# Kernel optimization log

Measured on AMD Instinct MI355X. Metric: run time of the kernel, lower is better.

The kernel has to match this reference:

```python
import jax, jax.numpy as jnp
import numpy as np

N = 50000
IN_CH = 128
OUT_CH = 64
H1, C1 = 8, 8


def gat_layer(x, src, dst, W, att_src, att_dst, bias, heads, out_ch, concat, n_nodes):
    # x: [N, F_in]; W: [F_in, heads*out_ch]; att_*: [heads, out_ch]; bias: [heads*out_ch] or [out_ch]
    h = (x @ W).reshape(n_nodes, heads, out_ch)              # [N,H,C]
    a_src = jnp.einsum('nhc,hc->nh', h, att_src)             # [N,H]
    a_dst = jnp.einsum('nhc,hc->nh', h, att_dst)             # [N,H]
    e = jax.nn.leaky_relu(a_src[src] + a_dst[dst], 0.2)      # [E,H]
    # segment softmax over incoming edges of each dst node
    m = jax.ops.segment_max(e, dst, num_segments=n_nodes)    # [N,H]
    p = jnp.exp(e - m[dst])                                  # [E,H]
    s = jax.ops.segment_sum(p, dst, num_segments=n_nodes)    # [N,H]
    alpha = p / (s[dst] + 1e-16)                             # [E,H]
    out = jax.ops.segment_sum(h[src] * alpha[:, :, None], dst, num_segments=n_nodes)  # [N,H,C]
    out = out.reshape(n_nodes, heads * out_ch) if concat else out.mean(axis=1)
    return out + bias


def setup_inputs() -> dict:
    key = jax.random.key(0)
    ks = jax.random.split(key, 12)
    E = 1600000
    x = jax.random.normal(ks[0], (N, IN_CH), dtype=jnp.float32)
    edge_index = jax.random.randint(ks[1], (2, E), 0, N, dtype=jnp.int64)
    sc = 0.1
    return {
        'x': x,
        'edge_index': edge_index,
        'W1': jax.random.normal(ks[2], (IN_CH, H1 * C1), dtype=jnp.float32) * sc,
        'att_src1': jax.random.normal(ks[3], (H1, C1), dtype=jnp.float32) * sc,
        'att_dst1': jax.random.normal(ks[4], (H1, C1), dtype=jnp.float32) * sc,
        'b1': jnp.zeros((H1 * C1,), dtype=jnp.float32),
        'W2': jax.random.normal(ks[5], (H1 * C1, OUT_CH), dtype=jnp.float32) * sc,
        'att_src2': jax.random.normal(ks[6], (1, OUT_CH), dtype=jnp.float32) * sc,
        'att_dst2': jax.random.normal(ks[7], (1, OUT_CH), dtype=jnp.float32) * sc,
        'b2': jnp.zeros((OUT_CH,), dtype=jnp.float32),
        'lin_W': jax.random.normal(ks[8], (OUT_CH, 1), dtype=jnp.float32) * sc,
        'lin_b': jnp.zeros((1,), dtype=jnp.float32),
    }


def reference(x, edge_index, W1, att_src1, att_dst1, b1, W2, att_src2, att_dst2, b2, lin_W, lin_b):
    # add self loops (PyG GATConv default)
    loops = jnp.arange(N, dtype=edge_index.dtype)
    src = jnp.concatenate([edge_index[0], loops])
    dst = jnp.concatenate([edge_index[1], loops])
    # dropout layers are identity in eval mode
    h = gat_layer(x, src, dst, W1, att_src1, att_dst1, b1, H1, C1, True, N)
    h = jax.nn.elu(h)
    h = gat_layer(h, src, dst, W2, att_src2, att_dst2, b2, 1, OUT_CH, False, N)
    return h @ lin_W + lin_b
```

## Files before the change

kernel.cpp:

```cpp
#include <hip/hip_runtime.h>
#include <hip/hip_bf16.h>
#include <math.h>

#define NN     50000
#define FIN    128
#define F1     64
#define NH1    8
#define F2     64

#define BSH    256
#define NB     ((NN + BSH - 1) / BSH)
#define BCAP   9472
#define PREB   13
#define MG1B   ((NN + 255) / 256)

typedef __bf16 bf16x8 __attribute__((ext_vector_type(8)));
typedef float  f32x4  __attribute__((ext_vector_type(4)));
typedef unsigned short u16x8 __attribute__((ext_vector_type(8)));


__device__ __forceinline__ float loadF(const void* p, long long i, int fp32) {
    if (fp32) return ((const float*)p)[i];
    return __bfloat162float(((const __hip_bfloat16*)p)[i]);
}
__device__ __forceinline__ int loadI_nt(const void* p, long long i, int i64) {
    if (i64) return (int)__builtin_nontemporal_load(&((const long long*)p)[i]);
    return __builtin_nontemporal_load(&((const int*)p)[i]);
}
__device__ __forceinline__ unsigned short f2bfu(float f) {
    unsigned u = __float_as_uint(f);
    return (unsigned short)((u + 0x7FFFu + ((u >> 16) & 1u)) >> 16);
}
__device__ __forceinline__ float b2f(unsigned short u) {
    return __uint_as_float(((unsigned)u) << 16);
}


__global__ __launch_bounds__(1024) void k_front(
    const void* __restrict__ x, const void* __restrict__ ei, int E, int Etot,
    int* __restrict__ flags,
    const void* __restrict__ W1, const void* __restrict__ W2,
    unsigned short* __restrict__ W1p, unsigned short* __restrict__ W2p,
    int* __restrict__ bcnt, unsigned* __restrict__ binned) {
    __shared__ int s_a, s_b;
    __shared__ int hist[NB], gbase[NB];
    int tid = threadIdx.x;
    if (blockIdx.x < PREB) {
        if (tid == 0) { s_a = 0; s_b = 0; }
        __syncthreads();
        const unsigned short* u = (const unsigned short*)x;
        int cnt = 0;
        for (int i = tid; i < 8192; i += 1024) {
            unsigned short v = u[i];
            if ((v & 0x7F80) == 0x7F80) cnt++;
        }
        if (cnt) atomicAdd(&s_a, cnt);
        const unsigned* e32 = (const unsigned*)ei;
        int nz = 0;
        for (int i = tid; i < 2048; i += 1024) {
            if (e32[2 * i + 1] != 0u) nz++;
        }
        if (nz) atomicAdd(&s_b, nz);
        __syncthreads();
        int fp32 = (s_a > 2) ? 1 : 0;
        if (tid == 0 && blockIdx.x == 0) {
            flags[0] = fp32;
            flags[1] = (s_b == 0) ? 1 : 0;
        }
        int gt = blockIdx.x * 1024 + tid, gs = PREB * 1024;
        for (int i = gt; i < (FIN / 32) * 4 * 512; i += gs) {
            int j = i & 7, l = (i >> 3) & 63, f = i >> 9;
            int kb = f >> 2, nt = f & 3;
            int k = kb * 32 + (l >> 4) * 8 + j, n = nt * 16 + (l & 15);
            W1p[i] = f2bfu(loadF(W1, k * 64 + n, fp32));
        }
        for (int i = gt; i < (F1 / 32) * 4 * 512; i += gs) {
            int j = i & 7, l = (i >> 3) & 63, f = i >> 9;
            int kb = f >> 2, nt = f & 3;
            int k = kb * 32 + (l >> 4) * 8 + j, n = nt * 16 + (l & 15);
            W2p[i] = f2bfu(loadF(W2, k * 64 + n, fp32));
        }
    } else {
        if (tid == 0) s_b = 0;
        for (int i = tid; i < NB; i += 1024) hist[i] = 0;
        __syncthreads();
        const unsigned* e32 = (const unsigned*)ei;
        int nz = 0;
        for (int i = tid; i < 2048; i += 1024) {
            if (e32[2 * i + 1] != 0u) nz++;
        }
        if (nz) atomicAdd(&s_b, nz);
        __syncthreads();
        int i64 = (s_b == 0) ? 1 : 0;
        long long base = (long long)(blockIdx.x - PREB) * 8192;
        unsigned pk[8]; short bb[8];
        #pragma unroll
        for (int u = 0; u < 8; ++u) {
            long long j = base + u * 1024 + tid;
            int s = -1, d = -1;
            if (j < Etot) {
                if (j < E) { s = loadI_nt(ei, j, i64); d = loadI_nt(ei, (long long)E + j, i64); }
                else       { s = d = (int)(j - E); }
            }
            if ((unsigned)s < NN && (unsigned)d < NN) {
                bb[u] = (short)(d >> 8);
                pk[u] = ((unsigned)s << 8) | (unsigned)(d & 255);
                atomicAdd(&hist[bb[u]], 1);
            } else bb[u] = -1;
        }
        __syncthreads();
        for (int i = tid; i < NB; i += 1024) {
            int h = hist[i];
            gbase[i] = h ? atomicAdd(&bcnt[i], h) : 0;
            hist[i] = 0;
        }
        __syncthreads();
        #pragma unroll
        for (int u = 0; u < 8; ++u) {
            if (bb[u] >= 0) {
                int pos = gbase[bb[u]] + atomicAdd(&hist[bb[u]], 1);
                if (pos < BCAP) binned[(size_t)bb[u] * BCAP + pos] = pk[u];
            }
        }
    }
}


__global__ __launch_bounds__(1024) void k_mid(
    const int* __restrict__ bcnt, const unsigned* __restrict__ binned,
    int* __restrict__ offs, int* __restrict__ perm,
    const void* __restrict__ x, const unsigned short* __restrict__ W1p,
    const void* __restrict__ attS, const void* __restrict__ attD,
    __hip_bfloat16* __restrict__ h1, float* __restrict__ a1s,
    float* __restrict__ a1d, const int* __restrict__ flags) {
    __shared__ __align__(16) char smem[33280];
    int tid = threadIdx.x;
    if (blockIdx.x < NB) {
        int* hist = (int*)smem;
        int* cur  = (int*)(smem + 1024);
        int* sd   = (int*)(smem + 2048);
        int bk = blockIdx.x;
        int n0 = bk * BSH;
        if (tid < 256) sd[tid] = (tid < NB) ? min(bcnt[tid], BCAP) : 0;
        __syncthreads();
        for (int off = 1; off < BSH; off <<= 1) {
            int t = 0;
            if (tid < 256 && tid >= off) t = sd[tid - off];
            __syncthreads();
            if (tid < 256) sd[tid] += t;
            __syncthreads();
        }
        int gb = (bk > 0) ? sd[bk - 1] : 0;
        if (bk == 0 && tid == 0) offs[NN] = sd[NB - 1];
        __syncthreads();
        int cnt = bcnt[bk]; if (cnt > BCAP) cnt = BCAP;
        const unsigned* bp = binned + (size_t)bk * BCAP;
        if (tid < 256) hist[tid] = 0;
        __syncthreads();
        for (int i = tid; i < cnt; i += 1024)
            atomicAdd(&hist[bp[i] & 255], 1);
        __syncthreads();
        int myh = (tid < 256) ? hist[tid] : 0;
        if (tid < 256) sd[tid] = myh;
        __syncthreads();
        for (int off = 1; off < BSH; off <<= 1) {
            int t = 0;
            if (tid < 256 && tid >= off) t = sd[tid - off];
            __syncthreads();
            if (tid < 256) sd[tid] += t;
            __syncthreads();
        }
        if (tid < 256) {
            int excl = sd[tid] - myh;
            cur[tid] = gb + excl;
            if (n0 + tid < NN) offs[n0 + tid] = gb + excl;
        }
        __syncthreads();
        for (int i = tid; i < cnt; i += 1024) {
            unsigned pk = bp[i];
            int pos = atomicAdd(&cur[pk & 255], 1);
            perm[pos] = (int)(pk >> 8);
        }
    } else {
        int fp32 = flags[0];
        unsigned short* hl = (unsigned short*)smem;
        float* attSl = (float*)(smem + 32768);
        float* attDl = (float*)(smem + 32768 + 256);
        if (tid < 64) { attSl[tid] = loadF(attS, tid, fp32); attDl[tid] = loadF(attD, tid, fp32); }
        int sub = tid >> 8, t = tid & 255;
        int w = t >> 6, l = t & 63;
        int quad = l >> 4, lm = l & 15;
        int n0 = (blockIdx.x - NB) * 256 + sub * 64;
        unsigned short* hls = hl + sub * 4096;

        bf16x8 bfr[16];
        #pragma unroll
        for (int f = 0; f < 16; ++f)
            bfr[f] = *(const bf16x8*)(W1p + f * 512 + l * 8);

        int nodeA = n0 + w * 16 + lm;
        long long rowA = (nodeA < NN) ? nodeA : 0;
        f32x4 acc[4];
        #pragma unroll
        for (int nt = 0; nt < 4; ++nt) acc[nt] = (f32x4){0.f, 0.f, 0.f, 0.f};

        #pragma unroll
        for (int kb = 0; kb < 4; ++kb) {
            bf16x8 af;
            if (!fp32) {
                af = *(const bf16x8*)((const unsigned short*)x + rowA * FIN + kb * 32 + quad * 8);
            } else {
                const float* xf = (const float*)x + rowA * FIN + kb * 32 + quad * 8;
                union { unsigned short s[8]; bf16x8 v; } tmp;
                #pragma unroll
                for (int j = 0; j < 8; ++j) tmp.s[j] = f2bfu(xf[j]);
                af = tmp.v;
            }
            #pragma unroll
            for (int nt = 0; nt < 4; ++nt)
                acc[nt] = __builtin_amdgcn_mfma_f32_16x16x32_bf16(af, bfr[kb * 4 + nt], acc[nt], 0, 0, 0);
        }

        #pragma unroll
        for (int nt = 0; nt < 4; ++nt) {
            #pragma unroll
            for (int r = 0; r < 4; ++r) {
                int nl = w * 16 + quad * 4 + r;
                int node = n0 + nl;
                int c = nt * 16 + lm;
                unsigned short hb = f2bfu(acc[nt][r]);
                hls[nl * 64 + c] = hb;
                if (node < NN) ((unsigned short*)h1)[(size_t)node * 64 + c] = hb;
            }
        }
        __syncthreads();
        #pragma unroll
        for (int pp = 0; pp < 2; ++pp) {
            int p = t + pp * 256;
            int nl = p >> 3, g = p & 7;
            int node = n0 + nl;
            float ss = 0.f, dd = 0.f;
            #pragma unroll
            for (int j = 0; j < 8; ++j) {
                float hv = b2f(hls[nl * 64 + g * 8 + j]);
                ss += hv * attSl[g * 8 + j];
                dd += hv * attDl[g * 8 + j];
            }
            if (node < NN) {
                a1s[(size_t)node * NH1 + g] = ss;
                a1d[(size_t)node * NH1 + g] = dd;
            }
        }
    }
}


#define HLP 72

__global__ __launch_bounds__(256) void k_agg1f(
    const int* __restrict__ offs, const int* __restrict__ perm,
    const __hip_bfloat16* __restrict__ h1, const float* __restrict__ a1s,
    const float* __restrict__ a1d, const void* __restrict__ b1,
    const unsigned short* __restrict__ W2p,
    const void* __restrict__ attS2, const void* __restrict__ attD2,
    const void* __restrict__ linW,
    float2* __restrict__ g2s, float* __restrict__ a2d,
    int n, const int* __restrict__ flags) {
    int fp32 = flags[0];
    __shared__ __align__(16) unsigned short hl[16 * HLP];
    __shared__ float attSl[64], attDl[64];
    __shared__ float sp[16 * 4], dp[16 * 4], gp[16 * 4];
    int tid = threadIdx.x;
    if (tid < 64) { attSl[tid] = loadF(attS2, tid, fp32); attDl[tid] = loadF(attD2, tid, fp32); }
    int w = tid >> 6, c = tid & 63;
    int n0 = blockIdx.x * 16;
    const unsigned short* hu = (const unsigned short*)h1;

    int g = c >> 3, q = c & 7;
    float b1r[8];
    #pragma unroll
    for (int k = 0; k < 8; ++k) b1r[k] = loadF(b1, q * 8 + k, fp32);

    for (int m = 0; m < 4; ++m) {
        int d = n0 + w * 4 + m;
        if (d < n) {
            int start = offs[d], end = offs[d + 1];
            float adl = a1d[(size_t)d * NH1 + q];
            float accv[8];
            #pragma unroll
            for (int k = 0; k < 8; ++k) accv[k] = 0.f;
            float den = 0.f;
            for (int i = start; i < end; i += 16) {
                int j0 = i + g, j1 = i + 8 + g;
                int jc0 = (j0 < end) ? j0 : (end - 1);
                int jc1 = (j1 < end) ? j1 : (end - 1);
                int sj0 = perm[jc0];
                int sj1 = perm[jc1];
                float as0 = a1s[(size_t)sj0 * NH1 + q];
                float as1 = a1s[(size_t)sj1 * NH1 + q];
                u16x8 hv0 = *(const u16x8*)(hu + (size_t)sj0 * 64 + q * 8);
                u16x8 hv1 = *(const u16x8*)(hu + (size_t)sj1 * 64 + q * 8);
                float e0 = as0 + adl;
                e0 = fmaxf(e0, 0.2f * e0);
                float p0 = (j0 < end) ? __expf(e0) : 0.f;
                float e1 = as1 + adl;
                e1 = fmaxf(e1, 0.2f * e1);
                float p1 = (j1 < end) ? __expf(e1) : 0.f;
                den += p0 + p1;
                #pragma unroll
                for (int k = 0; k < 8; ++k) {
                    accv[k] = fmaf(p0, b2f(hv0[k]), accv[k]);
                    accv[k] = fmaf(p1, b2f(hv1[k]), accv[k]);
                }
            }
            #pragma unroll
            for (int k = 0; k < 8; ++k) {
                accv[k] += __shfl_xor(accv[k], 8, 64);
                accv[k] += __shfl_xor(accv[k], 16, 64);
                accv[k] += __shfl_xor(accv[k], 32, 64);
            }
            den += __shfl_xor(den, 8, 64);
            den += __shfl_xor(den, 16, 64);
            den += __shfl_xor(den, 32, 64);
            float rden = 1.f / (den + 1e-16f);
            if (g == 0) {
                unsigned pk4[4];
                #pragma unroll
                for (int k = 0; k < 4; ++k) {
                    float v0 = fmaf(accv[2 * k],     rden, b1r[2 * k]);
                    float v1 = fmaf(accv[2 * k + 1], rden, b1r[2 * k + 1]);
                    v0 = (v0 > 0.f) ? v0 : expm1f(v0);
                    v1 = (v1 > 0.f) ? v1 : expm1f(v1);
                    pk4[k] = (unsigned)f2bfu(v0) | ((unsigned)f2bfu(v1) << 16);
                }
                *(uint4*)&hl[(w * 4 + m) * HLP + q * 8] =
                    make_uint4(pk4[0], pk4[1], pk4[2], pk4[3]);
            }
        }
    }
    __syncthreads();

    int quad = c >> 4, lm = c & 15;
    bf16x8 bf0 = *(const bf16x8*)(W2p + (0 * 4 + w) * 512 + c * 8);
    bf16x8 bf1 = *(const bf16x8*)(W2p + (1 * 4 + w) * 512 + c * 8);
    bf16x8 af0 = *(const bf16x8*)(hl + lm * HLP + 0 * 32 + quad * 8);
    bf16x8 af1 = *(const bf16x8*)(hl + lm * HLP + 1 * 32 + quad * 8);
    f32x4 acc2 = (f32x4){0.f, 0.f, 0.f, 0.f};
    acc2 = __builtin_amdgcn_mfma_f32_16x16x32_bf16(af0, bf0, acc2, 0, 0, 0);
    acc2 = __builtin_amdgcn_mfma_f32_16x16x32_bf16(af1, bf1, acc2, 0, 0, 0);

    int cg = w * 16 + lm;
    float aSc = attSl[cg], aDc = attDl[cg];
    float lWc = loadF(linW, cg, fp32);
    #pragma unroll
    for (int r = 0; r < 4; ++r) {
        int nl = quad * 4 + r;
        unsigned short hb = f2bfu(acc2[r]);
        float hv = b2f(hb);
        float pvs = hv * aSc, pvd = hv * aDc, pvg = hv * lWc;
        pvs += __shfl_xor(pvs, 1, 64); pvd += __shfl_xor(pvd, 1, 64); pvg += __shfl_xor(pvg, 1, 64);
        pvs += __shfl_xor(pvs, 2, 64); pvd += __shfl_xor(pvd, 2, 64); pvg += __shfl_xor(pvg, 2, 64);
        pvs += __shfl_xor(pvs, 4, 64); pvd += __shfl_xor(pvd, 4, 64); pvg += __shfl_xor(pvg, 4, 64);
        pvs += __shfl_xor(pvs, 8, 64); pvd += __shfl_xor(pvd, 8, 64); pvg += __shfl_xor(pvg, 8, 64);
        if (lm == 0) { sp[nl * 4 + w] = pvs; dp[nl * 4 + w] = pvd; gp[nl * 4 + w] = pvg; }
    }
    __syncthreads();
    if (tid < 16) {
        int node = n0 + tid;
        if (node < n) {
            float ss = sp[tid * 4 + 0] + sp[tid * 4 + 1] + sp[tid * 4 + 2] + sp[tid * 4 + 3];
            float dd = dp[tid * 4 + 0] + dp[tid * 4 + 1] + dp[tid * 4 + 2] + dp[tid * 4 + 3];
            float gg = gp[tid * 4 + 0] + gp[tid * 4 + 1] + gp[tid * 4 + 2] + gp[tid * 4 + 3];
            g2s[node] = make_float2(ss, gg);
            a2d[node] = dd;
        }
    }
}


__global__ __launch_bounds__(256) void k_agg2(
    const int* __restrict__ offs, const int* __restrict__ perm,
    const float2* __restrict__ g2s, const float* __restrict__ a2d,
    const void* __restrict__ b2, const void* __restrict__ linW,
    const void* __restrict__ linb,
    void* __restrict__ out, int n, const int* __restrict__ flags) {
    int fp32 = flags[0];
    int tid = threadIdx.x;
    int lane = tid & 63, wv = tid >> 6;
    int grp = lane >> 3, l8 = lane & 7;
    float cst = loadF(b2, lane, fp32) * loadF(linW, lane, fp32);
    #pragma unroll
    for (int off = 1; off < 64; off <<= 1) cst += __shfl_xor(cst, off, 64);
    cst += loadF(linb, 0, fp32);

    int d = blockIdx.x * 32 + wv * 8 + grp;
    if (d >= n) return;
    int start = offs[d], end = offs[d + 1];
    int last = end - 1;
    float ad = a2d[d];
    float acc = 0.f, den = 0.f;
    for (int i = start + l8; i < end; i += 16) {
        int j1 = i + 8;
        int s0 = perm[i];
        int s1 = perm[min(j1, last)];
        float2 ag0 = g2s[s0];
        float2 ag1 = g2s[s1];
        float e0 = ag0.x + ad;
        e0 = fmaxf(e0, 0.2f * e0);
        float p0 = __expf(e0);
        float e1 = ag1.x + ad;
        e1 = fmaxf(e1, 0.2f * e1);
        float p1 = (j1 <= last) ? __expf(e1) : 0.f;
        acc = fmaf(p0, ag0.y, acc);
        acc = fmaf(p1, ag1.y, acc);
        den += p0 + p1;
    }
    acc += __shfl_xor(acc, 1, 64); den += __shfl_xor(den, 1, 64);
    acc += __shfl_xor(acc, 2, 64); den += __shfl_xor(den, 2, 64);
    acc += __shfl_xor(acc, 4, 64); den += __shfl_xor(den, 4, 64);
    if (l8 == 0) {
        float r = acc / (den + 1e-16f) + cst;
        if (fp32) ((float*)out)[d] = r;
        else      ((__hip_bfloat16*)out)[d] = __float2bfloat16(r);
    }
}


static inline char* carve(char*& p, size_t bytes) {
    char* r = p;
    p += (bytes + 255) & ~size_t(255);
    return r;
}

extern "C" void kernel_launch(void* const* d_in, const int* in_sizes, int n_in,
                              void* d_out, int out_size, void* d_ws, size_t ws_size,
                              hipStream_t stream) {
    const void* x     = d_in[0];
    const void* ei    = d_in[1];
    const void* W1    = d_in[2];
    const void* attS1 = d_in[3];
    const void* attD1 = d_in[4];
    const void* b1    = d_in[5];
    const void* W2    = d_in[6];
    const void* attS2 = d_in[7];
    const void* attD2 = d_in[8];
    const void* b2    = d_in[9];
    const void* linW  = d_in[10];
    const void* linb  = d_in[11];

    int E    = in_sizes[1] / 2;
    int Etot = E + NN;

    char* p = (char*)d_ws;
    int*   flags = (int*)carve(p, 256);
    int*   bcnt  = (int*)carve(p, (size_t)NB * 4);
    unsigned short* W1p = (unsigned short*)carve(p, 8192 * 2);
    unsigned short* W2p = (unsigned short*)carve(p, 4096 * 2);
    int*   offs  = (int*)carve(p, (size_t)(NN + 1) * 4);
    int*   perm  = (int*)carve(p, (size_t)Etot * 4);
    unsigned* binned = (unsigned*)carve(p, (size_t)NB * BCAP * 4);
    float*    a1s    = (float*)carve(p, (size_t)NN * NH1 * 4);
    float*    a1d    = (float*)carve(p, (size_t)NN * NH1 * 4);
    __hip_bfloat16* h1 = (__hip_bfloat16*)carve(p, (size_t)NN * F1 * 2);
    float2* g2s = (float2*)carve(p, (size_t)NN * 8);
    float*  a2d = (float*)carve(p, (size_t)NN * 4);

    hipMemsetAsync(bcnt, 0, (size_t)NB * 4, stream);

    int nbin = (Etot + 8191) / 8192;
    k_front<<<PREB + nbin, 1024, 0, stream>>>(x, ei, E, Etot, flags,
                                              W1, W2, W1p, W2p, bcnt, binned);
    k_mid<<<NB + MG1B, 1024, 0, stream>>>(bcnt, binned, offs, perm,
                                          x, W1p, attS1, attD1, h1, a1s, a1d, flags);
    k_agg1f<<<(NN + 15) / 16, 256, 0, stream>>>(offs, perm, h1, a1s, a1d, b1,
                                                W2p, attS2, attD2, linW, g2s, a2d, NN, flags);
    k_agg2<<<(NN + 31) / 32, 256, 0, stream>>>(offs, perm, g2s, a2d, b2, linW, linb, d_out, NN, flags);
}
```

Baseline: 192.5 us.

## Replace two-level binned CSR build with global degree count and atomic placement

The CSR construction is reworked. Each edge's destination degree is now counted with a global atomic, a per-node prefix scan is done in k_mid, and a new k_place kernel rereads the edge list and scatters each source into perm with an atomic cursor per node. This removes the intermediate binned buffer and its capped bucket sort, and drops the BCAP truncation. In exchange it reads the edge indices a second time, adds an extra kernel launch, and issues about 1.65M global atomics on dcnt and on curs. The perm reads in the aggregation kernels also become nontemporal loads.

New measurement: 332.5 us. +72.7%, slower.

```diff
diff --git a/kernel.cpp b/kernel.cpp
--- a/kernel.cpp
+++ b/kernel.cpp
@@ -10,7 +10,6 @@
 
 #define BSH    256
 #define NB     ((NN + BSH - 1) / BSH)
-#define BCAP   9472
 #define PREB   13
 #define MG1B   ((NN + 255) / 256)
 
@@ -41,9 +40,9 @@
     int* __restrict__ flags,
     const void* __restrict__ W1, const void* __restrict__ W2,
     unsigned short* __restrict__ W1p, unsigned short* __restrict__ W2p,
-    int* __restrict__ bcnt, unsigned* __restrict__ binned) {
+    int* __restrict__ bcnt, int* __restrict__ dcnt) {
     __shared__ int s_a, s_b;
-    __shared__ int hist[NB], gbase[NB];
+    __shared__ int hist[NB];
     int tid = threadIdx.x;
     if (blockIdx.x < PREB) {
         if (tid == 0) { s_a = 0; s_b = 0; }
@@ -93,7 +92,6 @@
         __syncthreads();
         int i64 = (s_b == 0) ? 1 : 0;
         long long base = (long long)(blockIdx.x - PREB) * 8192;
-        unsigned pk[8]; short bb[8];
         #pragma unroll
         for (int u = 0; u < 8; ++u) {
             long long j = base + u * 1024 + tid;
@@ -103,32 +101,22 @@
                 else       { s = d = (int)(j - E); }
             }
             if ((unsigned)s < NN && (unsigned)d < NN) {
-                bb[u] = (short)(d >> 8);
-                pk[u] = ((unsigned)s << 8) | (unsigned)(d & 255);
-                atomicAdd(&hist[bb[u]], 1);
-            } else bb[u] = -1;
+                atomicAdd(&hist[d >> 8], 1);
+                atomicAdd(&dcnt[d], 1);
+            }
         }
         __syncthreads();
         for (int i = tid; i < NB; i += 1024) {
             int h = hist[i];
-            gbase[i] = h ? atomicAdd(&bcnt[i], h) : 0;
-            hist[i] = 0;
-        }
-        __syncthreads();
-        #pragma unroll
-        for (int u = 0; u < 8; ++u) {
-            if (bb[u] >= 0) {
-                int pos = gbase[bb[u]] + atomicAdd(&hist[bb[u]], 1);
-                if (pos < BCAP) binned[(size_t)bb[u] * BCAP + pos] = pk[u];
-            }
+            if (h) atomicAdd(&bcnt[i], h);
         }
     }
 }
 
 
 __global__ __launch_bounds__(1024) void k_mid(
-    const int* __restrict__ bcnt, const unsigned* __restrict__ binned,
-    int* __restrict__ offs, int* __restrict__ perm,
+    const int* __restrict__ bcnt, const int* __restrict__ dcnt,
+    int* __restrict__ offs, int* __restrict__ curs,
     const void* __restrict__ x, const unsigned short* __restrict__ W1p,
     const void* __restrict__ attS, const void* __restrict__ attD,
     __hip_bfloat16* __restrict__ h1, float* __restrict__ a1s,
@@ -136,12 +124,10 @@
     __shared__ __align__(16) char smem[33280];
     int tid = threadIdx.x;
     if (blockIdx.x < NB) {
-        int* hist = (int*)smem;
-        int* cur  = (int*)(smem + 1024);
-        int* sd   = (int*)(smem + 2048);
+        int* sd = (int*)smem;
         int bk = blockIdx.x;
         int n0 = bk * BSH;
-        if (tid < 256) sd[tid] = (tid < NB) ? min(bcnt[tid], BCAP) : 0;
+        if (tid < 256) sd[tid] = (tid < NB) ? bcnt[tid] : 0;
         __syncthreads();
         for (int off = 1; off < BSH; off <<= 1) {
             int t = 0;
@@ -153,14 +139,7 @@
         int gb = (bk > 0) ? sd[bk - 1] : 0;
         if (bk == 0 && tid == 0) offs[NN] = sd[NB - 1];
         __syncthreads();
-        int cnt = bcnt[bk]; if (cnt > BCAP) cnt = BCAP;
-        const unsigned* bp = binned + (size_t)bk * BCAP;
-        if (tid < 256) hist[tid] = 0;
-        __syncthreads();
-        for (int i = tid; i < cnt; i += 1024)
-            atomicAdd(&hist[bp[i] & 255], 1);
-        __syncthreads();
-        int myh = (tid < 256) ? hist[tid] : 0;
+        int myh = (tid < 256 && (n0 + tid) < NN) ? dcnt[n0 + tid] : 0;
         if (tid < 256) sd[tid] = myh;
         __syncthreads();
         for (int off = 1; off < BSH; off <<= 1) {
@@ -170,16 +149,10 @@
             if (tid < 256) sd[tid] += t;
             __syncthreads();
         }
-        if (tid < 256) {
-            int excl = sd[tid] - myh;
-            cur[tid] = gb + excl;
-            if (n0 + tid < NN) offs[n0 + tid] = gb + excl;
-        }
-        __syncthreads();
-        for (int i = tid; i < cnt; i += 1024) {
-            unsigned pk = bp[i];
-            int pos = atomicAdd(&cur[pk & 255], 1);
-            perm[pos] = (int)(pk >> 8);
+        if (tid < 256 && (n0 + tid) < NN) {
+            int e = gb + sd[tid] - myh;
+            offs[n0 + tid] = e;
+            curs[n0 + tid] = e;
         }
     } else {
         int fp32 = flags[0];
@@ -250,6 +223,38 @@
                 a1s[(size_t)node * NH1 + g] = ss;
                 a1d[(size_t)node * NH1 + g] = dd;
             }
+        }
+    }
+}
+
+
+__global__ __launch_bounds__(1024) void k_place(
+    const void* __restrict__ ei, int E, int Etot,
+    int* __restrict__ curs, int* __restrict__ perm) {
+    __shared__ int s_b;
+    int tid = threadIdx.x;
+    if (tid == 0) s_b = 0;
+    __syncthreads();
+    const unsigned* e32 = (const unsigned*)ei;
+    int nz = 0;
+    for (int i = tid; i < 2048; i += 1024) {
+        if (e32[2 * i + 1] != 0u) nz++;
+    }
+    if (nz) atomicAdd(&s_b, nz);
+    __syncthreads();
+    int i64 = (s_b == 0) ? 1 : 0;
+    long long base = (long long)blockIdx.x * 8192;
+    #pragma unroll
+    for (int u = 0; u < 8; ++u) {
+        long long j = base + u * 1024 + tid;
+        int s = -1, d = -1;
+        if (j < Etot) {
+            if (j < E) { s = loadI_nt(ei, j, i64); d = loadI_nt(ei, (long long)E + j, i64); }
+            else       { s = d = (int)(j - E); }
+        }
+        if ((unsigned)s < NN && (unsigned)d < NN) {
+            int pos = atomicAdd(&curs[d], 1);
+            perm[pos] = s;
         }
     }
 }
@@ -294,8 +299,8 @@
                 int j0 = i + g, j1 = i + 8 + g;
                 int jc0 = (j0 < end) ? j0 : (end - 1);
                 int jc1 = (j1 < end) ? j1 : (end - 1);
-                int sj0 = perm[jc0];
-                int sj1 = perm[jc1];
+                int sj0 = __builtin_nontemporal_load(&perm[jc0]);
+                int sj1 = __builtin_nontemporal_load(&perm[jc1]);
                 float as0 = a1s[(size_t)sj0 * NH1 + q];
                 float as1 = a1s[(size_t)sj1 * NH1 + q];
                 u16x8 hv0 = *(const u16x8*)(hu + (size_t)sj0 * 64 + q * 8);
@@ -401,8 +406,8 @@
     float acc = 0.f, den = 0.f;
     for (int i = start + l8; i < end; i += 16) {
         int j1 = i + 8;
-        int s0 = perm[i];
-        int s1 = perm[min(j1, last)];
+        int s0 = __builtin_nontemporal_load(&perm[i]);
+        int s1 = __builtin_nontemporal_load(&perm[min(j1, last)]);
         float2 ag0 = g2s[s0];
         float2 ag1 = g2s[s1];
         float e0 = ag0.x + ad;
@@ -454,24 +459,28 @@
     char* p = (char*)d_ws;
     int*   flags = (int*)carve(p, 256);
     int*   bcnt  = (int*)carve(p, (size_t)NB * 4);
+    int*   dcnt  = (int*)carve(p, (size_t)NN * 4);
+    int*   curs  = (int*)carve(p, (size_t)NN * 4);
     unsigned short* W1p = (unsigned short*)carve(p, 8192 * 2);
     unsigned short* W2p = (unsigned short*)carve(p, 4096 * 2);
     int*   offs  = (int*)carve(p, (size_t)(NN + 1) * 4);
     int*   perm  = (int*)carve(p, (size_t)Etot * 4);
-    unsigned* binned = (unsigned*)carve(p, (size_t)NB * BCAP * 4);
     float*    a1s    = (float*)carve(p, (size_t)NN * NH1 * 4);
     float*    a1d    = (float*)carve(p, (size_t)NN * NH1 * 4);
     __hip_bfloat16* h1 = (__hip_bfloat16*)carve(p, (size_t)NN * F1 * 2);
     float2* g2s = (float2*)carve(p, (size_t)NN * 8);
     float*  a2d = (float*)carve(p, (size_t)NN * 4);
 
-    hipMemsetAsync(bcnt, 0, (size_t)NB * 4, stream);
+    size_t zlen = (((size_t)NB * 4 + 255) & ~size_t(255)) +
+                  (((size_t)NN * 4 + 255) & ~size_t(255));
+    hipMemsetAsync(bcnt, 0, zlen, stream);
 
     int nbin = (Etot + 8191) / 8192;
     k_front<<<PREB + nbin, 1024, 0, stream>>>(x, ei, E, Etot, flags,
-                                              W1, W2, W1p, W2p, bcnt, binned);
-    k_mid<<<NB + MG1B, 1024, 0, stream>>>(bcnt, binned, offs, perm,
+                                              W1, W2, W1p, W2p, bcnt, dcnt);
+    k_mid<<<NB + MG1B, 1024, 0, stream>>>(bcnt, dcnt, offs, curs,
                                           x, W1p, attS1, attD1, h1, a1s, a1d, flags);
+    k_place<<<nbin, 1024, 0, stream>>>(ei, E, Etot, curs, perm);
     k_agg1f<<<(NN + 15) / 16, 256, 0, stream>>>(offs, perm, h1, a1s, a1d, b1,
                                                 W2p, attS2, attD2, linW, g2s, a2d, NN, flags);
     k_agg2<<<(NN + 31) / 32, 256, 0, stream>>>(offs, perm, g2s, a2d, b2, linW, linb, d_out, NN, flags);
```
